# Kernel tuning notes

Hardware: AMD Instinct MI355X
Metric: run time of the kernel (lower is better)

The kernel has to match this reference:

```python
import jax, jax.numpy as jnp
import numpy as np

VOCAB, EMB, HID = 5000, 16, 32
B, T = 256, 2048


def setup_inputs() -> dict:
    key = jax.random.key(0)
    k1, k2, k3, k4, k5 = jax.random.split(key, 5)
    tokens = jax.random.randint(k1, (B, T), 0, VOCAB, dtype=jnp.int32)
    emb = jax.random.normal(k2, (VOCAB, EMB), dtype=jnp.float32) * 0.05
    Wk = jax.random.normal(k3, (EMB, 4 * HID), dtype=jnp.float32) * 0.1
    Wr = jax.random.normal(k4, (HID, 4 * HID), dtype=jnp.float32) * 0.1
    b = jax.random.normal(k5, (4 * HID,), dtype=jnp.float32) * 0.1
    return {"tokens": tokens, "emb": emb, "Wk": Wk, "Wr": Wr, "b": b}


def reference(tokens, emb, Wk, Wr, b):
    # Embedding lookup: [B, T, EMB]
    x = emb[tokens]
    # Mask: Keras Masking on tiled token values -> masked where token == 0.
    mask = (tokens != 0)  # [B, T] True = valid step
    # Precompute input projections for all timesteps: [B, T, 4H]
    zx = jnp.einsum('bte,eh->bth', x, Wk) + b
    zx_t = jnp.swapaxes(zx, 0, 1)        # [T, B, 4H]
    mask_t = jnp.swapaxes(mask, 0, 1)    # [T, B]

    def step(carry, inp):
        h, c = carry
        z_x, m = inp
        z = z_x + h @ Wr                      # [B, 4H]
        i, f, g, o = jnp.split(z, 4, axis=-1) # Keras gate order i,f,g,o
        i = jax.nn.sigmoid(i)
        f = jax.nn.sigmoid(f)
        g = jnp.tanh(g)
        o = jax.nn.sigmoid(o)
        c_new = f * c + i * g
        h_new = o * jnp.tanh(c_new)
        m = m[:, None]
        # Keras masked RNN: masked steps carry forward previous state/output
        h = jnp.where(m, h_new, h)
        c = jnp.where(m, c_new, c)
        return (h, c), h

    h0 = jnp.zeros((tokens.shape[0], HID), dtype=zx.dtype)
    c0 = jnp.zeros((tokens.shape[0], HID), dtype=zx.dtype)
    _, hs = jax.lax.scan(step, (h0, c0), (zx_t, mask_t))
    return jnp.swapaxes(hs, 0, 1)  # [B, T, HID]
```

## Files before the change

### kernel.cpp

```cpp
#include <hip/hip_runtime.h>

#define G    128
#define HID  32
#define EMB  16
#define BB   256
#define TT   2048
#define VOC  5000

typedef float v2f __attribute__((ext_vector_type(2)));
typedef __attribute__((ext_vector_type(8))) short short8;
typedef __attribute__((ext_vector_type(4))) float f32x4;

__device__ __forceinline__ float bf2f(unsigned short u) {
    return __uint_as_float(((unsigned)u) << 16);
}
__device__ __forceinline__ unsigned short f2bf(float f) {
    unsigned x = __float_as_uint(f);
    return (unsigned short)((x + 0x7FFFu + ((x >> 16) & 1u)) >> 16);
}
__device__ __forceinline__ float sigm(float x) {
    const float e = __expf(-x);
    return __builtin_amdgcn_rcpf(1.f + e);
}
__device__ __forceinline__ float tanh_f(float x) {
    const float e = __expf(-2.f * x);
    return (1.f - e) * __builtin_amdgcn_rcpf(1.f + e);
}
__device__ __forceinline__ float rdlf(float v, int k) {
    return __int_as_float(__builtin_amdgcn_readlane(__float_as_int(v), k));
}
template <int CTRL>
__device__ __forceinline__ unsigned dppq_u(unsigned v) {
    return (unsigned)__builtin_amdgcn_update_dpp(0, (int)v, CTRL, 0xF, 0xF, true);
}
template <int CTRL>
__device__ __forceinline__ float dppq_f(float v) {
    return __uint_as_float(dppq_u<CTRL>(__float_as_uint(v)));
}
#define DPP_XOR1 0xB1
#define DPP_XOR2 0x4E

__device__ __host__ __forceinline__ int col_a(int l) {
    return (l >> 1) + 32 * (l & 1);
}

__global__ void detect_kernel(const unsigned int* __restrict__ bias_w,
                              int* __restrict__ flag) {
    if (threadIdx.x == 0 && blockIdx.x == 0) {
        bool evens_zero = true, anybig = false;
        for (int i = 0; i < 64; ++i) {
            const unsigned u  = bias_w[i];
            const unsigned lo = u & 0xFFFFu;
            const float vlo = __uint_as_float(lo << 16);
            const float vhi = __uint_as_float(u & 0xFFFF0000u);
            if (lo != 0u) evens_zero = false;
            if (!(fabsf(vlo) < 1e6f) || !(fabsf(vhi) < 1e6f)) anybig = true;
        }
        *flag = (evens_zero || anybig) ? 1 : 0;
    }
}

__global__ __launch_bounds__(64) void zk_kernel(
    const void* __restrict__ emb, const void* __restrict__ Wk,
    const void* __restrict__ bias, float* __restrict__ ZK,
    const int* __restrict__ flag)
{
    const int l = threadIdx.x;
    const int v = blockIdx.x;
    const bool f32 = flag[0] != 0;
    const int ca = col_a(l), cb = ca + 64;

    float x[EMB], wa[EMB], wb[EMB], ba, bb;
    if (f32) {
        const float* E = (const float*)emb + (size_t)v * EMB;
        const float* W = (const float*)Wk;
        const float* B = (const float*)bias;
#pragma unroll
        for (int e = 0; e < EMB; ++e) {
            x[e]  = E[e];
            wa[e] = W[e * G + ca];
            wb[e] = W[e * G + cb];
        }
        ba = B[ca]; bb = B[cb];
    } else {
        const unsigned short* E = (const unsigned short*)emb + (size_t)v * EMB;
        const unsigned short* W = (const unsigned short*)Wk;
        const unsigned short* B = (const unsigned short*)bias;
#pragma unroll
        for (int e = 0; e < EMB; ++e) {
            x[e]  = bf2f(E[e]);
            wa[e] = bf2f(W[e * G + ca]);
            wb[e] = bf2f(W[e * G + cb]);
        }
        ba = bf2f(B[ca]); bb = bf2f(B[cb]);
    }
    float za = ba, zb = bb;
#pragma unroll
    for (int e = 0; e < EMB; ++e) {
        za = fmaf(x[e], wa[e], za);
        zb = fmaf(x[e], wb[e], zb);
    }
    ZK[(size_t)v * G + 2 * l]     = za;
    ZK[(size_t)v * G + 2 * l + 1] = zb;
}

template <bool F32OUT>
__device__ __forceinline__ void scan_zk_loop(
    const int* __restrict__ trow, const float* __restrict__ ZK,
    void* __restrict__ orow, const short8 (&Bf)[8], int lane)
{
    const bool  h0  = (lane & 1) == 0;
    const float zsc = h0 ? 2.f : 1.f, gm = h0 ? 2.f : 1.f, ga = h0 ? -1.f : 0.f;
    const int   oj  = lane >> 1;
    const int   g4  = (lane >> 4) & 3;
    const bool  u_odd = (lane >> 1) & 1;
    int badr[4];
#pragma unroll
    for (int q = 0; q < 4; ++q) badr[q] = 64 * (lane >> 4) + 16 * q;

    const f32x4 zc = {0.f, 0.f, 0.f, 0.f};
    float h = 0.f, c = 0.f;

    int tcur[16], tnxt[16];
#pragma unroll
    for (int p = 0; p < 16; ++p) tcur[p] = trow[p];
#pragma unroll
    for (int p = 0; p < 16; ++p) tnxt[p] = trow[16 + p];

    v2f pz[4];
#pragma unroll
    for (int d = 0; d < 4; ++d)
        pz[d] = *(const v2f*)(ZK + (size_t)tcur[d] * G + 2 * lane);

    for (int cc = 0; cc < TT / 16; ++cc) {
        const int base = cc * 16;
#pragma unroll
        for (int u = 0; u < 16; ++u) {
            const int t = base + u;
            const v2f z = pz[u & 3];
            {
                const int ptok = (u + 4 < 16) ? tcur[u + 4] : tnxt[u + 4 - 16];
                pz[u & 3] = *(const v2f*)(ZK + (size_t)ptok * G + 2 * lane);
            }

            const unsigned rh  = __float_as_uint(h) + 0x8000u;
            const unsigned prt = dppq_u<DPP_XOR2>(rh);
            const unsigned plo = u_odd ? prt : rh;
            const unsigned phi = u_odd ? rh : prt;
            const unsigned pair = __builtin_amdgcn_perm(phi, plo, 0x07060302u);
            union { unsigned u4[4]; short8 s8; } au;
#pragma unroll
            for (int q = 0; q < 4; ++q)
                au.u4[q] = (unsigned)__builtin_amdgcn_ds_bpermute(badr[q], (int)pair);
            const short8 Af = au.s8;

            f32x4 d0 = __builtin_amdgcn_mfma_f32_16x16x32_bf16(Af, Bf[0], zc, 0, 0, 0);
            f32x4 d1 = __builtin_amdgcn_mfma_f32_16x16x32_bf16(Af, Bf[1], zc, 0, 0, 0);
            f32x4 d2 = __builtin_amdgcn_mfma_f32_16x16x32_bf16(Af, Bf[2], zc, 0, 0, 0);
            f32x4 d3 = __builtin_amdgcn_mfma_f32_16x16x32_bf16(Af, Bf[3], zc, 0, 0, 0);
            f32x4 d4 = __builtin_amdgcn_mfma_f32_16x16x32_bf16(Af, Bf[4], zc, 0, 0, 0);
            f32x4 d5 = __builtin_amdgcn_mfma_f32_16x16x32_bf16(Af, Bf[5], zc, 0, 0, 0);
            f32x4 d6 = __builtin_amdgcn_mfma_f32_16x16x32_bf16(Af, Bf[6], zc, 0, 0, 0);
            f32x4 d7 = __builtin_amdgcn_mfma_f32_16x16x32_bf16(Af, Bf[7], zc, 0, 0, 0);

            const float mva = (g4 < 2) ? (g4 == 0 ? d0.x : d1.x)
                                       : (g4 == 2 ? d2.x : d3.x);
            const float mvb = (g4 < 2) ? (g4 == 0 ? d4.x : d5.x)
                                       : (g4 == 2 ? d6.x : d7.x);
            const float za = z.x + mva;
            const float zb = z.y + mvb;

            const float aa1 = sigm(za);
            const float s2  = sigm(zb * zsc);
            const float aa2 = fmaf(s2, gm, ga);
            const float x1  = dppq_f<DPP_XOR1>(aa1);
            const float x2  = dppq_f<DPP_XOR1>(aa2);
            const float iV = h0 ? aa1 : x1, fV = h0 ? x1 : aa1;
            const float gV = h0 ? aa2 : x2, oV = h0 ? x2 : aa2;
            const float cN = fmaf(fV, c, iV * gV);
            const float hN = oV * tanh_f(cN);
            const bool  m  = tcur[u] != 0;
            c = m ? cN : c;
            h = m ? hN : h;

            const int oi = t * HID + oj;
            if (F32OUT) __builtin_nontemporal_store(h, (float*)orow + oi);
            else        __builtin_nontemporal_store(f2bf(h), (unsigned short*)orow + oi);
        }
#pragma unroll
        for (int p = 0; p < 16; ++p) tcur[p] = tnxt[p];
        const int nb = (cc + 2) * 16;
        if (nb <= TT - 16) {
#pragma unroll
            for (int p = 0; p < 16; ++p) tnxt[p] = trow[nb + p];
        }
    }
}

__global__ __launch_bounds__(64) void scan_zk_kernel(
    const int* __restrict__ tokens, const float* __restrict__ ZK,
    const void* __restrict__ Wr, const void* __restrict__ bias,
    void* __restrict__ out, const int* __restrict__ flag)
{
    const int lane = threadIdx.x, b = blockIdx.x;
    const bool f32 = flag[0] != 0;

    short8 Bf[8];
    const int n  = lane & 15;
    const int k0 = (lane >> 4) * 8;
#pragma unroll
    for (int p = 0; p < 8; ++p) {
        const int ell = 16 * (p & 3) + n;
        const int col = (p < 4) ? col_a(ell) : (col_a(ell) + 64);
        short el[8];
        if (f32) {
            const float* W = (const float*)Wr;
#pragma unroll
            for (int j = 0; j < 8; ++j) el[j] = (short)f2bf(W[(k0 + j) * G + col]);
        } else {
            const unsigned short* W = (const unsigned short*)Wr;
#pragma unroll
            for (int j = 0; j < 8; ++j) el[j] = (short)W[(k0 + j) * G + col];
        }
        short8 s;
#pragma unroll
        for (int j = 0; j < 8; ++j) s[j] = el[j];
        Bf[p] = s;
    }

    const int* trow = tokens + (size_t)b * TT;
    if (f32) scan_zk_loop<true >(trow, ZK, (char*)out + (size_t)b * TT * HID * 4, Bf, lane);
    else     scan_zk_loop<false>(trow, ZK, (char*)out + (size_t)b * TT * HID * 2, Bf, lane);
}

template <bool F32>
__device__ __forceinline__ void row_load(const void* emb, int tok, uint4* r) {
    if (F32) { const uint4* p = (const uint4*)((const float*)emb + (size_t)tok*EMB);
               r[0]=p[0]; r[1]=p[1]; r[2]=p[2]; r[3]=p[3]; }
    else     { const uint4* p = (const uint4*)((const unsigned short*)emb + (size_t)tok*EMB);
               r[0]=p[0]; r[1]=p[1]; }
}
template <bool F32>
__device__ __forceinline__ void row_unpack(const uint4* r, float* x) {
    if (F32) {
        const unsigned w[16] = {r[0].x,r[0].y,r[0].z,r[0].w, r[1].x,r[1].y,r[1].z,r[1].w,
                                r[2].x,r[2].y,r[2].z,r[2].w, r[3].x,r[3].y,r[3].z,r[3].w};
#pragma unroll
        for (int e = 0; e < 16; ++e) x[e] = __uint_as_float(w[e]);
    } else {
        const unsigned w[8] = {r[0].x,r[0].y,r[0].z,r[0].w, r[1].x,r[1].y,r[1].z,r[1].w};
#pragma unroll
        for (int q = 0; q < 8; ++q) {
            x[2*q]   = __uint_as_float(w[q] << 16);
            x[2*q+1] = __uint_as_float(w[q] & 0xFFFF0000u);
        }
    }
}

template <bool F32>
__device__ __forceinline__ void scan_fused_loop(
    const int* __restrict__ trow, const void* __restrict__ emb, void* orow,
    const float (&wka)[EMB], const float (&wkb)[EMB],
    const float (&wra)[HID], const float (&wrb)[HID],
    float za0, float zb0, const int* tl, int lane)
{
    const bool  lo  = lane < HID;
    const float zsc = lo ? 2.f : 1.f, gm = lo ? 2.f : 1.f, ga = lo ? -1.f : 0.f;
    float h = 0.f, c = 0.f;
    uint4 praw[2][4];
    row_load<F32>(emb, trow[0], praw[0]);
    row_load<F32>(emb, trow[1], praw[1]);

    for (int tt = 0; tt < TT; tt += 2) {
#pragma unroll
        for (int u = 0; u < 2; ++u) {
            const int t = tt + u;
            float x[EMB];
            row_unpack<F32>(praw[u], x);
            int tn = t + 2; tn = tn > TT - 1 ? TT - 1 : tn;
            row_load<F32>(emb, tl[tn], praw[u]);
            float za = za0, zb = zb0;
#pragma unroll
            for (int e = 0; e < EMB; ++e) { za = fmaf(x[e], wka[e], za); zb = fmaf(x[e], wkb[e], zb); }
#pragma unroll
            for (int k = 0; k < HID; ++k) {
                const float hk = rdlf(h, k);
                za = fmaf(hk, wra[k], za);
                zb = fmaf(hk, wrb[k], zb);
            }
            const float a1 = sigm(za);
            const float s2 = sigm(zb * zsc);
            const float a2 = fmaf(s2, gm, ga);
            const float x1 = __shfl_xor(a1, 32);
            const float x2 = __shfl_xor(a2, 32);
            const float iV = lo ? a1 : x1, fV = lo ? x1 : a1;
            const float gV = lo ? a2 : x2, oV = lo ? x2 : a2;
            const float cN = fmaf(fV, c, iV * gV);
            const float hN = oV * tanh_f(cN);
            const bool  m  = tl[t] != 0;
            c = m ? cN : c;
            h = m ? hN : h;
            const int oi = t * HID + (lane & (HID - 1));
            if (F32) ((float*)orow)[oi] = h;
            else     ((unsigned short*)orow)[oi] = f2bf(h);
        }
    }
}

__global__ __launch_bounds__(64) void scan_fused_kernel(
    const int* __restrict__ tokens, const void* __restrict__ emb,
    const void* __restrict__ Wk, const void* __restrict__ Wr,
    const void* __restrict__ bias, void* __restrict__ out,
    const int* __restrict__ flag, int defmode)
{
    __shared__ int tl[TT];
    const int lane = threadIdx.x, b = blockIdx.x;
    const bool f32 = flag ? (flag[0] != 0) : (defmode != 0);
    const int* trow = tokens + (size_t)b * TT;
    for (int t = lane; t < TT; t += 64) tl[t] = trow[t];

    float wka[EMB], wkb[EMB], wra[HID], wrb[HID], za0, zb0;
    if (f32) {
        const float* WK = (const float*)Wk; const float* WR = (const float*)Wr;
        const float* B  = (const float*)bias;
#pragma unroll
        for (int e = 0; e < EMB; ++e) { wka[e] = WK[e*G + lane]; wkb[e] = WK[e*G + lane + 64]; }
#pragma unroll
        for (int k = 0; k < HID; ++k) { wra[k] = WR[k*G + lane]; wrb[k] = WR[k*G + lane + 64]; }
        za0 = B[lane]; zb0 = B[lane + 64];
    } else {
        const unsigned short* WK = (const unsigned short*)Wk;
        const unsigned short* WR = (const unsigned short*)Wr;
        const unsigned short* B  = (const unsigned short*)bias;
#pragma unroll
        for (int e = 0; e < EMB; ++e) { wka[e] = bf2f(WK[e*G + lane]); wkb[e] = bf2f(WK[e*G + lane + 64]); }
#pragma unroll
        for (int k = 0; k < HID; ++k) { wra[k] = bf2f(WR[k*G + lane]); wrb[k] = bf2f(WR[k*G + lane + 64]); }
        za0 = bf2f(B[lane]); zb0 = bf2f(B[lane + 64]);
    }
    __syncthreads();

    if (f32) scan_fused_loop<true >(trow, emb, (char*)out + (size_t)b*TT*HID*4,
                                    wka, wkb, wra, wrb, za0, zb0, tl, lane);
    else     scan_fused_loop<false>(trow, emb, (char*)out + (size_t)b*TT*HID*2,
                                    wka, wkb, wra, wrb, za0, zb0, tl, lane);
}

extern "C" void kernel_launch(void* const* d_in, const int* in_sizes, int n_in,
                              void* d_out, int out_size, void* d_ws, size_t ws_size,
                              hipStream_t stream) {
    const int*  tokens = (const int*)d_in[0];
    const void* emb    = d_in[1];
    const void* Wk     = d_in[2];
    const void* Wr     = d_in[3];
    const void* bias   = d_in[4];

    const size_t zk_off   = 256;
    const size_t zk_bytes = (size_t)VOC * G * sizeof(float);

    if (ws_size >= zk_off + zk_bytes) {
        int*   flag = (int*)d_ws;
        float* ZK   = (float*)((char*)d_ws + zk_off);
        detect_kernel<<<1, 64, 0, stream>>>((const unsigned int*)bias, flag);
        zk_kernel<<<VOC, 64, 0, stream>>>(emb, Wk, bias, ZK, flag);
        scan_zk_kernel<<<BB, 64, 0, stream>>>(tokens, ZK, Wr, bias, d_out, flag);
    } else if (ws_size >= 16) {
        int* flag = (int*)d_ws;
        detect_kernel<<<1, 64, 0, stream>>>((const unsigned int*)bias, flag);
        scan_fused_kernel<<<BB, 64, 0, stream>>>(tokens, emb, Wk, Wr, bias, d_out, flag, 1);
    } else {
        scan_fused_kernel<<<BB, 64, 0, stream>>>(tokens, emb, Wk, Wr, bias, d_out, nullptr, 1);
    }
}
```

Baseline: 534.3 us.

## Fold log2e into weights, use exp2, replace bpermute with DPP lane shuffles

Pre-scales the ZK table and recurrent weights by log2(e) so the gate sigmoids can call the hardware exp2 directly instead of __expf, which removes a multiply from the serial recurrence. The four ds_bpermute operations that build the MFMA A operand become the original value plus three DPP row permutes (half-mirror, rotate-by-8, mirror), and the weight K-index is XOR-permuted to match the new lane order. The aim is to shorten the per-timestep latency chain by avoiding LDS-path permutes. The detect kernel is also made wave-parallel with ballots. Rounding the log2e-scaled weights to bf16 changes numerics slightly, and the permutation bookkeeping is easy to get wrong.

```diff
diff --git a/kernel.cpp b/kernel.cpp
--- a/kernel.cpp
+++ b/kernel.cpp
@@ -7,6 +7,9 @@
 #define TT   2048
 #define VOC  5000
 
+#define LOG2E      1.44269504088896340736f
+#define NEG2LOG2E -2.88539008177792681472f
+
 typedef float v2f __attribute__((ext_vector_type(2)));
 typedef __attribute__((ext_vector_type(8))) short short8;
 typedef __attribute__((ext_vector_type(4))) float f32x4;
@@ -18,6 +21,14 @@
     unsigned x = __float_as_uint(f);
     return (unsigned short)((x + 0x7FFFu + ((x >> 16) & 1u)) >> 16);
 }
+__device__ __forceinline__ float sigm2(float x) {
+    const float e = __builtin_amdgcn_exp2f(-x);
+    return __builtin_amdgcn_rcpf(1.f + e);
+}
+__device__ __forceinline__ float tanh_n(float x) {
+    const float e = __builtin_amdgcn_exp2f(x * NEG2LOG2E);
+    return (1.f - e) * __builtin_amdgcn_rcpf(1.f + e);
+}
 __device__ __forceinline__ float sigm(float x) {
     const float e = __expf(-x);
     return __builtin_amdgcn_rcpf(1.f + e);
@@ -37,27 +48,30 @@
 __device__ __forceinline__ float dppq_f(float v) {
     return __uint_as_float(dppq_u<CTRL>(__float_as_uint(v)));
 }
-#define DPP_XOR1 0xB1
-#define DPP_XOR2 0x4E
+#define DPP_XOR1   0xB1
+#define DPP_XOR2   0x4E
+#define DPP_HMIRR  0x141
+#define DPP_ROR8   0x128
+#define DPP_MIRR   0x140
 
 __device__ __host__ __forceinline__ int col_a(int l) {
     return (l >> 1) + 32 * (l & 1);
 }
 
-__global__ void detect_kernel(const unsigned int* __restrict__ bias_w,
-                              int* __restrict__ flag) {
-    if (threadIdx.x == 0 && blockIdx.x == 0) {
-        bool evens_zero = true, anybig = false;
-        for (int i = 0; i < 64; ++i) {
-            const unsigned u  = bias_w[i];
-            const unsigned lo = u & 0xFFFFu;
-            const float vlo = __uint_as_float(lo << 16);
-            const float vhi = __uint_as_float(u & 0xFFFF0000u);
-            if (lo != 0u) evens_zero = false;
-            if (!(fabsf(vlo) < 1e6f) || !(fabsf(vhi) < 1e6f)) anybig = true;
-        }
-        *flag = (evens_zero || anybig) ? 1 : 0;
-    }
+__global__ __launch_bounds__(64) void detect_kernel(
+    const unsigned int* __restrict__ bias_w, int* __restrict__ flag)
+{
+    const int l = threadIdx.x;
+    const unsigned u  = bias_w[l];
+    const unsigned lo = u & 0xFFFFu;
+    const float vlo = __uint_as_float(lo << 16);
+    const float vhi = __uint_as_float(u & 0xFFFF0000u);
+    const bool nz_even = (lo != 0u);
+    const bool big = !(fabsf(vlo) < 1e6f) || !(fabsf(vhi) < 1e6f);
+    const unsigned long long nz = __ballot(nz_even);
+    const unsigned long long bg = __ballot(big);
+    if (l == 0 && blockIdx.x == 0)
+        *flag = (nz == 0ull || bg != 0ull) ? 1 : 0;
 }
 
 __global__ __launch_bounds__(64) void zk_kernel(
@@ -100,8 +114,8 @@
         za = fmaf(x[e], wa[e], za);
         zb = fmaf(x[e], wb[e], zb);
     }
-    ZK[(size_t)v * G + 2 * l]     = za;
-    ZK[(size_t)v * G + 2 * l + 1] = zb;
+    ZK[(size_t)v * G + 2 * l]     = za * LOG2E;
+    ZK[(size_t)v * G + 2 * l + 1] = zb * LOG2E;
 }
 
 template <bool F32OUT>
@@ -114,9 +128,6 @@
     const int   oj  = lane >> 1;
     const int   g4  = (lane >> 4) & 3;
     const bool  u_odd = (lane >> 1) & 1;
-    int badr[4];
-#pragma unroll
-    for (int q = 0; q < 4; ++q) badr[q] = 64 * (lane >> 4) + 16 * q;
 
     const f32x4 zc = {0.f, 0.f, 0.f, 0.f};
     float h = 0.f, c = 0.f;
@@ -148,10 +159,11 @@
             const unsigned plo = u_odd ? prt : rh;
             const unsigned phi = u_odd ? rh : prt;
             const unsigned pair = __builtin_amdgcn_perm(phi, plo, 0x07060302u);
+            const unsigned q1 = dppq_u<DPP_HMIRR>(pair);
+            const unsigned q2 = dppq_u<DPP_ROR8 >(pair);
+            const unsigned q3 = dppq_u<DPP_MIRR >(pair);
             union { unsigned u4[4]; short8 s8; } au;
-#pragma unroll
-            for (int q = 0; q < 4; ++q)
-                au.u4[q] = (unsigned)__builtin_amdgcn_ds_bpermute(badr[q], (int)pair);
+            au.u4[0] = pair; au.u4[1] = q1; au.u4[2] = q2; au.u4[3] = q3;
             const short8 Af = au.s8;
 
             f32x4 d0 = __builtin_amdgcn_mfma_f32_16x16x32_bf16(Af, Bf[0], zc, 0, 0, 0);
@@ -170,15 +182,15 @@
             const float za = z.x + mva;
             const float zb = z.y + mvb;
 
-            const float aa1 = sigm(za);
-            const float s2  = sigm(zb * zsc);
+            const float aa1 = sigm2(za);
+            const float s2  = sigm2(zb * zsc);
             const float aa2 = fmaf(s2, gm, ga);
             const float x1  = dppq_f<DPP_XOR1>(aa1);
             const float x2  = dppq_f<DPP_XOR1>(aa2);
             const float iV = h0 ? aa1 : x1, fV = h0 ? x1 : aa1;
             const float gV = h0 ? aa2 : x2, oV = h0 ? x2 : aa2;
             const float cN = fmaf(fV, c, iV * gV);
-            const float hN = oV * tanh_f(cN);
+            const float hN = oV * tanh_n(cN);
             const bool  m  = tcur[u] != 0;
             c = m ? cN : c;
             h = m ? hN : h;
@@ -212,15 +224,18 @@
     for (int p = 0; p < 8; ++p) {
         const int ell = 16 * (p & 3) + n;
         const int col = (p < 4) ? col_a(ell) : (col_a(ell) + 64);
+        const int jx  = (p & 3) << 1;
         short el[8];
         if (f32) {
             const float* W = (const float*)Wr;
 #pragma unroll
-            for (int j = 0; j < 8; ++j) el[j] = (short)f2bf(W[(k0 + j) * G + col]);
+            for (int j = 0; j < 8; ++j)
+                el[j] = (short)f2bf(W[(k0 + (j ^ jx)) * G + col] * LOG2E);
         } else {
             const unsigned short* W = (const unsigned short*)Wr;
 #pragma unroll
-            for (int j = 0; j < 8; ++j) el[j] = (short)W[(k0 + j) * G + col];
+            for (int j = 0; j < 8; ++j)
+                el[j] = (short)f2bf(bf2f(W[(k0 + (j ^ jx)) * G + col]) * LOG2E);
         }
         short8 s;
 #pragma unroll
```

Result: faster. 439.6 us (-17.7%).
